# Kernel optimization log

Hardware: AMD Instinct MI355X
Metric: run time of the kernel (lower is better)

Reference implementation:

```python
import jax, jax.numpy as jnp
import numpy as np

N_ENTITIES = 100000
N_RELATIONS = 64
EMBED_DIM = 128
BATCH = 16384
KG_L2_LAMBDA = 1e-05


def setup_inputs() -> dict:
    key = jax.random.key(0)
    ks = jax.random.split(key, 8)
    d = EMBED_DIM
    scale = 1.0 / np.sqrt(d)  # xavier-ish init scale
    return {
        'h': jax.random.randint(ks[0], (BATCH,), 0, N_ENTITIES),
        'r': jax.random.randint(ks[1], (BATCH,), 0, N_RELATIONS),
        'pos_t': jax.random.randint(ks[2], (BATCH,), 0, N_ENTITIES),
        'neg_t': jax.random.randint(ks[3], (BATCH,), 0, N_ENTITIES),
        'entity_embed': jax.random.normal(ks[4], (N_ENTITIES, d), jnp.float32) * scale,
        'relation_embed': jax.random.normal(ks[5], (N_RELATIONS, d), jnp.float32) * scale,
        'h_trans_w1': jnp.ones((d,), jnp.float32),
        'h_trans_w2': jnp.ones((d,), jnp.float32),
        'h_bias_b': jnp.zeros((d,), jnp.float32),
        'r_trans_w1': jnp.ones((d,), jnp.float32),
        'r_trans_w2': jnp.ones((d,), jnp.float32),
        'r_bias_b': jnp.zeros((d,), jnp.float32),
        'sem_trans_w': jax.random.normal(ks[6], (2 * d, d), jnp.float32) * scale,
    }


def _l2_loss_mean(x):
    return jnp.mean(jnp.sum(x * x, axis=1) / 2.0)


def reference(h, r, pos_t, neg_t, entity_embed, relation_embed,
              h_trans_w1, h_trans_w2, h_bias_b,
              r_trans_w1, r_trans_w2, r_bias_b, sem_trans_w):
    h_e = entity_embed[h]          # (B, d)
    r_e = relation_embed[r]        # (B, d)
    pos_t_e = entity_embed[pos_t]  # (B, d)
    neg_t_e = entity_embed[neg_t]  # (B, d)

    # calc_sur: sem[b,i,j] = h_e[b,i] * r_e[b,j]; matmul(sem, w) == h_e * (r_e @ w),
    # matmul(sem^T, w) == r_e * (h_e @ w). Fused form of the same math.
    r_w1 = (r_e @ h_trans_w1)[:, None]
    r_w2 = (r_e @ h_trans_w2)[:, None]
    h_w1 = (h_e @ r_trans_w1)[:, None]
    h_w2 = (h_e @ r_trans_w2)[:, None]
    cross_h = h_e * r_w1 + r_e * h_w2 + h_bias_b  # (B, d)
    cross_r = h_e * r_w2 + r_e * h_w1 + r_bias_b  # (B, d)

    pred_t = jnp.concatenate([cross_h, cross_r], axis=1) @ sem_trans_w  # (B, d)
    pos_score = jnp.sum(pred_t * pos_t_e, axis=1)
    neg_score = jnp.sum(pred_t * neg_t_e, axis=1)
    # -logsigmoid(x) == softplus(-x)
    kg_loss = jnp.mean(jax.nn.softplus(-(pos_score - neg_score)))
    l2_loss = (_l2_loss_mean(cross_h) + _l2_loss_mean(cross_r)
               + _l2_loss_mean(pos_t_e) + _l2_loss_mean(neg_t_e))
    return kg_loss + KG_L2_LAMBDA * l2_loss
```

## Files before the change

kernel.cpp:

```cpp
#include <hip/hip_runtime.h>
#include <hip/hip_bf16.h>

#define B_TOTAL 16384
#define EMB 128
#define NBLK 256
#define TPB 256
#define KG_LAMBDA 1e-5f
#define WT_STRIDE 264

typedef float f32x4 __attribute__((ext_vector_type(4)));
typedef unsigned u32x4 __attribute__((ext_vector_type(4)));
typedef __bf16 bf16x8 __attribute__((ext_vector_type(8)));

__device__ __forceinline__ unsigned pack_bf16x2(float a, float b) {
  unsigned ua = __float_as_uint(a);
  unsigned ub = __float_as_uint(b);
  ua = (ua + 0x7fffu + ((ua >> 16) & 1u)) >> 16;
  ub = (ub + 0x7fffu + ((ub >> 16) & 1u)) >> 16;
  return ua | (ub << 16);
}

__global__ __launch_bounds__(TPB, 2) void sur_fused(
    const int* __restrict__ h, const int* __restrict__ r,
    const int* __restrict__ pos_t, const int* __restrict__ neg_t,
    const float* __restrict__ ent, const float* __restrict__ rel,
    const float* __restrict__ htw1, const float* __restrict__ htw2,
    const float* __restrict__ hbias,
    const float* __restrict__ rtw1, const float* __restrict__ rtw2,
    const float* __restrict__ rbias,
    const float* __restrict__ W, float* __restrict__ partials) {
  __shared__ __align__(16) unsigned short Wt[128][WT_STRIDE];
  __shared__ float svec[6 * 128];
  __shared__ float redbuf[2][4];

  const int tid = threadIdx.x;
  const int lane = tid & 63;
  const int wave = tid >> 6;
  const int ri = lane & 15;
  const int q = lane >> 4;

  for (int idx = tid; idx < 16384; idx += TPB) {
    const int c = idx & 127;
    const int kp = idx >> 7;
    const int k = kp * 2;
    const float f0 = W[k * EMB + c];
    const float f1 = W[(k + 1) * EMB + c];
    *reinterpret_cast<unsigned*>(&Wt[c][k]) = pack_bf16x2(f0, f1);
  }
  for (int i = tid; i < 768; i += TPB) {
    const int v = i >> 7, c = i & 127;
    const float* src = v == 0 ? htw1 : v == 1 ? htw2 : v == 2 ? hbias
                     : v == 3 ? rtw1 : v == 4 ? rtw2 : rbias;
    svec[i] = src[c];
  }
  __syncthreads();

  const int rowbase = blockIdx.x * 64 + wave * 16;
  const int hoff = h[rowbase + ri] * EMB;
  const int roff = r[rowbase + ri] * EMB;

  float he[4][8], re[4][8];
  #pragma unroll
  for (int kt = 0; kt < 4; ++kt) {
    const int c0 = kt * 32 + q * 8;
    const float4 a0 = *reinterpret_cast<const float4*>(ent + hoff + c0);
    const float4 a1 = *reinterpret_cast<const float4*>(ent + hoff + c0 + 4);
    const float4 b0 = *reinterpret_cast<const float4*>(rel + roff + c0);
    const float4 b1 = *reinterpret_cast<const float4*>(rel + roff + c0 + 4);
    he[kt][0] = a0.x; he[kt][1] = a0.y; he[kt][2] = a0.z; he[kt][3] = a0.w;
    he[kt][4] = a1.x; he[kt][5] = a1.y; he[kt][6] = a1.z; he[kt][7] = a1.w;
    re[kt][0] = b0.x; re[kt][1] = b0.y; re[kt][2] = b0.z; re[kt][3] = b0.w;
    re[kt][4] = b1.x; re[kt][5] = b1.y; re[kt][6] = b1.z; re[kt][7] = b1.w;
  }

  float prw1 = 0.f, prw2 = 0.f, phw1 = 0.f, phw2 = 0.f;
  #pragma unroll
  for (int kt = 0; kt < 4; ++kt) {
    const int c0 = kt * 32 + q * 8;
    #pragma unroll
    for (int j = 0; j < 8; ++j) {
      prw1 = fmaf(re[kt][j], svec[0 * 128 + c0 + j], prw1);
      prw2 = fmaf(re[kt][j], svec[1 * 128 + c0 + j], prw2);
      phw1 = fmaf(he[kt][j], svec[3 * 128 + c0 + j], phw1);
      phw2 = fmaf(he[kt][j], svec[4 * 128 + c0 + j], phw2);
    }
  }
  prw1 += __shfl_xor(prw1, 16); prw2 += __shfl_xor(prw2, 16);
  phw1 += __shfl_xor(phw1, 16); phw2 += __shfl_xor(phw2, 16);
  prw1 += __shfl_xor(prw1, 32); prw2 += __shfl_xor(prw2, 32);
  phw1 += __shfl_xor(phw1, 32); phw2 += __shfl_xor(phw2, 32);

  float acc_l2 = 0.f;
  u32x4 afu[8];
  #pragma unroll
  for (int kt = 0; kt < 4; ++kt) {
    const int c0 = kt * 32 + q * 8;
    float ch[8], cr[8];
    #pragma unroll
    for (int j = 0; j < 8; ++j) {
      const float hb = svec[2 * 128 + c0 + j];
      const float rb = svec[5 * 128 + c0 + j];
      ch[j] = fmaf(he[kt][j], prw1, fmaf(re[kt][j], phw2, hb));
      cr[j] = fmaf(he[kt][j], prw2, fmaf(re[kt][j], phw1, rb));
      acc_l2 += ch[j] * ch[j] + cr[j] * cr[j];
    }
    #pragma unroll
    for (int d = 0; d < 4; ++d) {
      afu[kt][d]     = pack_bf16x2(ch[2 * d], ch[2 * d + 1]);
      afu[kt + 4][d] = pack_bf16x2(cr[2 * d], cr[2 * d + 1]);
    }
  }

  int pidx[4], nidx[4];
  #pragma unroll
  for (int g = 0; g < 4; ++g) {
    pidx[g] = pos_t[rowbase + q * 4 + g] * EMB;
    nidx[g] = neg_t[rowbase + q * 4 + g] * EMB;
  }
  float pe[4][8], ne[4][8];
  #pragma unroll
  for (int g = 0; g < 4; ++g) {
    #pragma unroll
    for (int n = 0; n < 8; ++n) {
      pe[g][n] = ent[pidx[g] + n * 16 + ri];
      ne[g][n] = ent[nidx[g] + n * 16 + ri];
    }
  }

  f32x4 acc[8];
  #pragma unroll
  for (int n = 0; n < 8; ++n) acc[n] = 0.f;
  #pragma unroll
  for (int t = 0; t < 8; ++t) {
    const bf16x8 av = __builtin_bit_cast(bf16x8, afu[t]);
    #pragma unroll
    for (int n = 0; n < 8; ++n) {
      const bf16x8 bv = *reinterpret_cast<const bf16x8*>(&Wt[n * 16 + ri][t * 32 + q * 8]);
      acc[n] = __builtin_amdgcn_mfma_f32_16x16x32_bf16(av, bv, acc[n], 0, 0, 0);
    }
  }

  float sp[4] = {0.f, 0.f, 0.f, 0.f}, sn[4] = {0.f, 0.f, 0.f, 0.f};
  #pragma unroll
  for (int n = 0; n < 8; ++n) {
    #pragma unroll
    for (int g = 0; g < 4; ++g) {
      sp[g] = fmaf(acc[n][g], pe[g][n], sp[g]);
      sn[g] = fmaf(acc[n][g], ne[g][n], sn[g]);
      acc_l2 += pe[g][n] * pe[g][n] + ne[g][n] * ne[g][n];
    }
  }
  #pragma unroll
  for (int m = 1; m < 16; m <<= 1) {
    #pragma unroll
    for (int g = 0; g < 4; ++g) {
      sp[g] += __shfl_xor(sp[g], m);
      sn[g] += __shfl_xor(sn[g], m);
    }
  }
  float acc_kg = 0.f;
  if (ri == 0) {
    #pragma unroll
    for (int g = 0; g < 4; ++g) {
      const float x = sn[g] - sp[g];
      acc_kg += fmaxf(x, 0.f) + log1pf(expf(-fabsf(x)));
    }
  }

  float kg = acc_kg, l2 = acc_l2;
  #pragma unroll
  for (int m = 1; m < 64; m <<= 1) {
    kg += __shfl_xor(kg, m);
    l2 += __shfl_xor(l2, m);
  }
  if (lane == 0) { redbuf[0][wave] = kg; redbuf[1][wave] = l2; }
  __syncthreads();
  if (tid == 0) {
    float K = 0.f, L = 0.f;
    #pragma unroll
    for (int w = 0; w < 4; ++w) { K += redbuf[0][w]; L += redbuf[1][w]; }
    partials[2 * blockIdx.x] = K;
    partials[2 * blockIdx.x + 1] = L;
  }
}

__global__ void sur_finalize(const float* __restrict__ partials,
                             float* __restrict__ out) {
  const int t = threadIdx.x;
  float kg = 0.f, l2 = 0.f;
  for (int i = t; i < NBLK; i += 256) {
    kg += partials[2 * i];
    l2 += partials[2 * i + 1];
  }
  #pragma unroll
  for (int m = 1; m < 64; m <<= 1) {
    kg += __shfl_xor(kg, m);
    l2 += __shfl_xor(l2, m);
  }
  __shared__ float s[2][4];
  const int w = t >> 6, lane = t & 63;
  if (lane == 0) { s[0][w] = kg; s[1][w] = l2; }
  __syncthreads();
  if (t == 0) {
    const float K = s[0][0] + s[0][1] + s[0][2] + s[0][3];
    const float L = s[1][0] + s[1][1] + s[1][2] + s[1][3];
    out[0] = K / (float)B_TOTAL + KG_LAMBDA * (0.5f * L / (float)B_TOTAL);
  }
}

extern "C" void kernel_launch(void* const* d_in, const int* in_sizes, int n_in,
                              void* d_out, int out_size, void* d_ws, size_t ws_size,
                              hipStream_t stream) {
  const int* h     = (const int*)d_in[0];
  const int* r     = (const int*)d_in[1];
  const int* pos_t = (const int*)d_in[2];
  const int* neg_t = (const int*)d_in[3];
  const float* ent  = (const float*)d_in[4];
  const float* rel  = (const float*)d_in[5];
  const float* htw1 = (const float*)d_in[6];
  const float* htw2 = (const float*)d_in[7];
  const float* hb   = (const float*)d_in[8];
  const float* rtw1 = (const float*)d_in[9];
  const float* rtw2 = (const float*)d_in[10];
  const float* rb   = (const float*)d_in[11];
  const float* W    = (const float*)d_in[12];
  float* partials = (float*)d_ws;
  float* out = (float*)d_out;

  hipLaunchKernelGGL(sur_fused, dim3(NBLK), dim3(TPB), 0, stream,
                     h, r, pos_t, neg_t, ent, rel,
                     htw1, htw2, hb, rtw1, rtw2, rb, W, partials);
  hipLaunchKernelGGL(sur_finalize, dim3(1), dim3(256), 0, stream, partials, out);
}
```

Baseline: 118.2 us.

## Precompute bf16 weight image once and replace finalize kernel with atomics

Adds a prep kernel that transposes and packs W to bf16, together with the small weight vectors, into a padded workspace image. Each main block then streams that image into LDS with coalesced float4 copies, where before all 256 blocks did strided fp32 loads and packing. The embedding gathers are issued before the barrier so they overlap the LDS fill. The finalize kernel is removed: each block atomically adds its scaled partial into the output after a memset. This adds a memset and a launch and makes the float sum order nondeterministic.

```diff
diff --git a/kernel.cpp b/kernel.cpp
--- a/kernel.cpp
+++ b/kernel.cpp
@@ -7,6 +7,10 @@
 #define TPB 256
 #define KG_LAMBDA 1e-5f
 #define WT_STRIDE 264
+#define IMG_BYTES 73728
+#define IMG_DW (IMG_BYTES / 4)
+#define WT_DW 16896
+#define SVEC_BYTE_OFF 67584
 
 typedef float f32x4 __attribute__((ext_vector_type(4)));
 typedef unsigned u32x4 __attribute__((ext_vector_type(4)));
@@ -20,18 +24,46 @@
   return ua | (ub << 16);
 }
 
+__global__ __launch_bounds__(256) void sur_prep(
+    const float* __restrict__ W,
+    const float* __restrict__ htw1, const float* __restrict__ htw2,
+    const float* __restrict__ hbias,
+    const float* __restrict__ rtw1, const float* __restrict__ rtw2,
+    const float* __restrict__ rbias,
+    unsigned* __restrict__ img) {
+  const int idx = blockIdx.x * 256 + threadIdx.x;
+  if (idx < WT_DW) {
+    const int c = idx / 132;
+    const int kp = idx - c * 132;
+    unsigned v = 0;
+    if (kp < 128) {
+      const float f0 = W[(2 * kp) * EMB + c];
+      const float f1 = W[(2 * kp + 1) * EMB + c];
+      v = pack_bf16x2(f0, f1);
+    }
+    img[idx] = v;
+  } else {
+    const int j = idx - WT_DW;
+    float val = 0.f;
+    if (j < 768) {
+      const int vsel = j >> 7, cc = j & 127;
+      const float* src = vsel == 0 ? htw1 : vsel == 1 ? htw2 : vsel == 2 ? hbias
+                       : vsel == 3 ? rtw1 : vsel == 4 ? rtw2 : rbias;
+      val = src[cc];
+    }
+    img[idx] = __float_as_uint(val);
+  }
+}
+
 __global__ __launch_bounds__(TPB, 2) void sur_fused(
     const int* __restrict__ h, const int* __restrict__ r,
     const int* __restrict__ pos_t, const int* __restrict__ neg_t,
     const float* __restrict__ ent, const float* __restrict__ rel,
-    const float* __restrict__ htw1, const float* __restrict__ htw2,
-    const float* __restrict__ hbias,
-    const float* __restrict__ rtw1, const float* __restrict__ rtw2,
-    const float* __restrict__ rbias,
-    const float* __restrict__ W, float* __restrict__ partials) {
-  __shared__ __align__(16) unsigned short Wt[128][WT_STRIDE];
-  __shared__ float svec[6 * 128];
+    const unsigned* __restrict__ img, float* __restrict__ out) {
+  __shared__ __align__(16) unsigned char smem[IMG_BYTES];
   __shared__ float redbuf[2][4];
+  unsigned short (*Wt)[WT_STRIDE] = (unsigned short(*)[WT_STRIDE])smem;
+  const float* svec = (const float*)(smem + SVEC_BYTE_OFF);
 
   const int tid = threadIdx.x;
   const int lane = tid & 63;
@@ -39,39 +71,49 @@
   const int ri = lane & 15;
   const int q = lane >> 4;
 
-  for (int idx = tid; idx < 16384; idx += TPB) {
-    const int c = idx & 127;
-    const int kp = idx >> 7;
-    const int k = kp * 2;
-    const float f0 = W[k * EMB + c];
-    const float f1 = W[(k + 1) * EMB + c];
-    *reinterpret_cast<unsigned*>(&Wt[c][k]) = pack_bf16x2(f0, f1);
-  }
-  for (int i = tid; i < 768; i += TPB) {
-    const int v = i >> 7, c = i & 127;
-    const float* src = v == 0 ? htw1 : v == 1 ? htw2 : v == 2 ? hbias
-                     : v == 3 ? rtw1 : v == 4 ? rtw2 : rbias;
-    svec[i] = src[c];
-  }
-  __syncthreads();
-
   const int rowbase = blockIdx.x * 64 + wave * 16;
-  const int hoff = h[rowbase + ri] * EMB;
-  const int roff = r[rowbase + ri] * EMB;
+  const int hidx = h[rowbase + ri] * EMB;
+  const int ridx = r[rowbase + ri] * EMB;
+  int pidx[4], nidx[4];
+  #pragma unroll
+  for (int g = 0; g < 4; ++g) {
+    pidx[g] = pos_t[rowbase + q * 4 + g] * EMB;
+    nidx[g] = neg_t[rowbase + q * 4 + g] * EMB;
+  }
+
+  {
+    const float4* gsrc = (const float4*)img;
+    float4* ldst = (float4*)smem;
+    #pragma unroll
+    for (int i = 0; i < IMG_BYTES / 16 / TPB; ++i)
+      ldst[i * TPB + tid] = gsrc[i * TPB + tid];
+  }
 
   float he[4][8], re[4][8];
   #pragma unroll
   for (int kt = 0; kt < 4; ++kt) {
     const int c0 = kt * 32 + q * 8;
-    const float4 a0 = *reinterpret_cast<const float4*>(ent + hoff + c0);
-    const float4 a1 = *reinterpret_cast<const float4*>(ent + hoff + c0 + 4);
-    const float4 b0 = *reinterpret_cast<const float4*>(rel + roff + c0);
-    const float4 b1 = *reinterpret_cast<const float4*>(rel + roff + c0 + 4);
+    const float4 a0 = *reinterpret_cast<const float4*>(ent + hidx + c0);
+    const float4 a1 = *reinterpret_cast<const float4*>(ent + hidx + c0 + 4);
+    const float4 b0 = *reinterpret_cast<const float4*>(rel + ridx + c0);
+    const float4 b1 = *reinterpret_cast<const float4*>(rel + ridx + c0 + 4);
     he[kt][0] = a0.x; he[kt][1] = a0.y; he[kt][2] = a0.z; he[kt][3] = a0.w;
     he[kt][4] = a1.x; he[kt][5] = a1.y; he[kt][6] = a1.z; he[kt][7] = a1.w;
     re[kt][0] = b0.x; re[kt][1] = b0.y; re[kt][2] = b0.z; re[kt][3] = b0.w;
     re[kt][4] = b1.x; re[kt][5] = b1.y; re[kt][6] = b1.z; re[kt][7] = b1.w;
   }
+
+  float pe[4][8], ne[4][8];
+  #pragma unroll
+  for (int g = 0; g < 4; ++g) {
+    #pragma unroll
+    for (int n = 0; n < 8; ++n) {
+      pe[g][n] = ent[pidx[g] + n * 16 + ri];
+      ne[g][n] = ent[nidx[g] + n * 16 + ri];
+    }
+  }
+
+  __syncthreads();
 
   float prw1 = 0.f, prw2 = 0.f, phw1 = 0.f, phw2 = 0.f;
   #pragma unroll
@@ -111,22 +153,6 @@
     }
   }
 
-  int pidx[4], nidx[4];
-  #pragma unroll
-  for (int g = 0; g < 4; ++g) {
-    pidx[g] = pos_t[rowbase + q * 4 + g] * EMB;
-    nidx[g] = neg_t[rowbase + q * 4 + g] * EMB;
-  }
-  float pe[4][8], ne[4][8];
-  #pragma unroll
-  for (int g = 0; g < 4; ++g) {
-    #pragma unroll
-    for (int n = 0; n < 8; ++n) {
-      pe[g][n] = ent[pidx[g] + n * 16 + ri];
-      ne[g][n] = ent[nidx[g] + n * 16 + ri];
-    }
-  }
-
   f32x4 acc[8];
   #pragma unroll
   for (int n = 0; n < 8; ++n) acc[n] = 0.f;
@@ -176,35 +202,9 @@
   if (lane == 0) { redbuf[0][wave] = kg; redbuf[1][wave] = l2; }
   __syncthreads();
   if (tid == 0) {
-    float K = 0.f, L = 0.f;
-    #pragma unroll
-    for (int w = 0; w < 4; ++w) { K += redbuf[0][w]; L += redbuf[1][w]; }
-    partials[2 * blockIdx.x] = K;
-    partials[2 * blockIdx.x + 1] = L;
-  }
-}
-
-__global__ void sur_finalize(const float* __restrict__ partials,
-                             float* __restrict__ out) {
-  const int t = threadIdx.x;
-  float kg = 0.f, l2 = 0.f;
-  for (int i = t; i < NBLK; i += 256) {
-    kg += partials[2 * i];
-    l2 += partials[2 * i + 1];
-  }
-  #pragma unroll
-  for (int m = 1; m < 64; m <<= 1) {
-    kg += __shfl_xor(kg, m);
-    l2 += __shfl_xor(l2, m);
-  }
-  __shared__ float s[2][4];
-  const int w = t >> 6, lane = t & 63;
-  if (lane == 0) { s[0][w] = kg; s[1][w] = l2; }
-  __syncthreads();
-  if (t == 0) {
-    const float K = s[0][0] + s[0][1] + s[0][2] + s[0][3];
-    const float L = s[1][0] + s[1][1] + s[1][2] + s[1][3];
-    out[0] = K / (float)B_TOTAL + KG_LAMBDA * (0.5f * L / (float)B_TOTAL);
+    const float K = redbuf[0][0] + redbuf[0][1] + redbuf[0][2] + redbuf[0][3];
+    const float L = redbuf[1][0] + redbuf[1][1] + redbuf[1][2] + redbuf[1][3];
+    atomicAdd(out, (K + KG_LAMBDA * 0.5f * L) * (1.0f / (float)B_TOTAL));
   }
 }
 
@@ -224,11 +224,12 @@
   const float* rtw2 = (const float*)d_in[10];
   const float* rb   = (const float*)d_in[11];
   const float* W    = (const float*)d_in[12];
-  float* partials = (float*)d_ws;
+  unsigned* img = (unsigned*)d_ws;
   float* out = (float*)d_out;
 
+  hipMemsetAsync(d_out, 0, sizeof(float), stream);
+  hipLaunchKernelGGL(sur_prep, dim3(IMG_DW / 256), dim3(256), 0, stream,
+                     W, htw1, htw2, hb, rtw1, rtw2, rb, img);
   hipLaunchKernelGGL(sur_fused, dim3(NBLK), dim3(TPB), 0, stream,
-                     h, r, pos_t, neg_t, ent, rel,
-                     htw1, htw2, hb, rtw1, rtw2, rb, W, partials);
-  hipLaunchKernelGGL(sur_finalize, dim3(1), dim3(256), 0, stream, partials, out);
-}
+                     h, r, pos_t, neg_t, ent, rel, img, out);
+}
```

Result: no change. 116.1 us (-1.8%).
